# Performance work log

Measured on AMD Instinct MI355X. Metric: run time of the kernel, lower is better.

Reference implementation:

```python
import jax, jax.numpy as jnp
import numpy as np

B, S, D, H = 8, 2048, 1024, 1024

def setup_inputs() -> dict:
    key = jax.random.key(0)
    ks = jax.random.split(key, 7)
    scale = 1.0 / np.sqrt(D)
    x = jax.random.normal(ks[0], (B, S, D), dtype=jnp.float32)
    W_q = jax.random.uniform(ks[1], (H, D), jnp.float32, -scale, scale)
    b_q = jax.random.uniform(ks[2], (H,), jnp.float32, -scale, scale)
    W_k = jax.random.uniform(ks[3], (H, D), jnp.float32, -scale, scale)
    b_k = jax.random.uniform(ks[4], (H,), jnp.float32, -scale, scale)
    W_v = jax.random.uniform(ks[5], (H, D), jnp.float32, -scale, scale)
    b_v = jax.random.uniform(ks[6], (H,), jnp.float32, -scale, scale)
    return {"x": x, "W_q": W_q, "b_q": b_q, "W_k": W_k, "b_k": b_k, "W_v": W_v, "b_v": b_v}

def reference(x, W_q, b_q, W_k, b_k, W_v, b_v):
    # Linear layers: y = x @ W.T + b (torch nn.Linear convention)
    q = jnp.einsum('bsd,hd->bsh', x, W_q) + b_q
    k = jnp.einsum('bsd,hd->bsh', x, W_k) + b_k
    v = jnp.einsum('bsd,hd->bsh', x, W_v) + b_v
    score = jnp.einsum('bqh,bkh->bqk', q, k) / jnp.sqrt(jnp.float32(H))
    causal = jnp.tril(jnp.ones((S, S), dtype=bool))  # lower-triangular mask
    score = jnp.where(causal, score, jnp.float32(-1e9))
    attn = jax.nn.softmax(score, axis=-1)
    return jnp.einsum('bqk,bkh->bqh', attn, v)
```

## Files before the change

kernel.cpp:

```cpp
#include <hip/hip_runtime.h>
#include <hip/hip_bf16.h>
#include <cstdint>

#define BB 8
#define SS 2048
#define DD 1024
#define HH 1024

typedef __bf16 bf16x8 __attribute__((ext_vector_type(8)));
typedef float f32x4 __attribute__((ext_vector_type(4)));

#define AS1C(p) ((const __attribute__((address_space(1))) void*)(p))
#define AS3(p)  ((__attribute__((address_space(3))) void*)(p))

__device__ __forceinline__ float bf2f(uint16_t h) {
  union { uint32_t u; float f; } v; v.u = ((uint32_t)h) << 16; return v.f;
}
__device__ __forceinline__ uint16_t f2bf(float f) {
  union { float f; uint32_t u; } v; v.f = f;
  uint32_t u = v.u;
  return (uint16_t)((u + 0x7FFFu + ((u >> 16) & 1u)) >> 16);
}

__global__ void cvt_f32_bf16(const float* __restrict__ src,
                             uint16_t* __restrict__ dst, int n) {
  int i = (blockIdx.x * blockDim.x + threadIdx.x) * 8;
  const int stride = gridDim.x * blockDim.x * 8;
  for (; i < n; i += stride) {
    float4 f0 = *(const float4*)(src + i);
    float4 f1 = *(const float4*)(src + i + 4);
    alignas(16) uint16_t o[8];
    o[0] = f2bf(f0.x); o[1] = f2bf(f0.y); o[2] = f2bf(f0.z); o[3] = f2bf(f0.w);
    o[4] = f2bf(f1.x); o[5] = f2bf(f1.y); o[6] = f2bf(f1.z); o[7] = f2bf(f1.w);
    *(uint4*)(dst + i) = *(const uint4*)o;
  }
}

__global__ void cvt3_f32_bf16(const float* __restrict__ s0, const float* __restrict__ s1,
                              const float* __restrict__ s2, uint16_t* __restrict__ d0,
                              uint16_t* __restrict__ d1, uint16_t* __restrict__ d2, int n) {
  const float* src = (blockIdx.y == 0) ? s0 : (blockIdx.y == 1) ? s1 : s2;
  uint16_t* dst = (blockIdx.y == 0) ? d0 : (blockIdx.y == 1) ? d1 : d2;
  int i = (blockIdx.x * blockDim.x + threadIdx.x) * 8;
  const int stride = gridDim.x * blockDim.x * 8;
  for (; i < n; i += stride) {
    float4 f0 = *(const float4*)(src + i);
    float4 f1 = *(const float4*)(src + i + 4);
    alignas(16) uint16_t o[8];
    o[0] = f2bf(f0.x); o[1] = f2bf(f0.y); o[2] = f2bf(f0.z); o[3] = f2bf(f0.w);
    o[4] = f2bf(f1.x); o[5] = f2bf(f1.y); o[6] = f2bf(f1.z); o[7] = f2bf(f1.w);
    *(uint4*)(dst + i) = *(const uint4*)o;
  }
}

template <int MODE>
__launch_bounds__(256, 2)
__global__ void gemm_bt(const uint16_t* __restrict__ Aroot,
                        const uint16_t* __restrict__ Broot,
                        const float* __restrict__ bias,
                        void* __restrict__ Croot) {
  constexpr int K   = (MODE == 3) ? 2048 : 1024;
  constexpr int LDA = (MODE == 3) ? 2048 : 1024;
  constexpr int LDB = (MODE == 3) ? 2048 : 1024;
  constexpr int LDC = (MODE == 2) ? 2048 : 1024;

  const int tm = blockIdx.x, tn = blockIdx.y;
  if constexpr (MODE == 2) { if (tn > tm) return; }

  const uint16_t* A = Aroot;
  const uint16_t* Bp = Broot;
  uint16_t* C16 = (uint16_t*)Croot;
  float*    C32 = (float*)Croot;
  if constexpr (MODE == 2) {
    size_t z = blockIdx.z;
    A  += z * (size_t)(SS * DD);
    Bp += z * (size_t)(SS * DD);
    C16 += z * (size_t)SS * (size_t)SS;
  }
  if constexpr (MODE == 3) {
    size_t z = blockIdx.z;
    A  += z * (size_t)SS * (size_t)SS;
    Bp += z * (size_t)(HH * SS);
    C32 += z * (size_t)(SS * HH);
  }

  const int m0 = tm * 128, n0 = tn * 128;
  int kmax = K;
  if constexpr (MODE == 3) {
    kmax = (tm + 1) * 128;
    if (kmax > K) kmax = K;
  }

  __shared__ uint16_t As[128 * 32];
  __shared__ uint16_t Bs[128 * 32];

  const int tid  = threadIdx.x;
  const int lane = tid & 63;
  const int wv   = tid >> 6;
  const int wm   = (wv & 1) * 64;
  const int wn   = (wv >> 1) * 64;

  f32x4 acc[4][4];
#pragma unroll
  for (int i = 0; i < 4; i++)
#pragma unroll
    for (int j = 0; j < 4; j++)
#pragma unroll
      for (int e = 0; e < 4; e++) acc[i][j][e] = 0.f;

  const int lrow = lane >> 2;
  const int lcol = (lane & 3) * 8;
  const int r0   = wv * 32;

  const uint16_t* gA = A + (size_t)(m0 + r0 + lrow) * LDA + lcol;
  const uint16_t* gB = Bp + (size_t)(n0 + r0 + lrow) * LDB + lcol;

  const int fr = lane & 15;
  const int fk = (lane >> 4) * 8;

  for (int k0 = 0; k0 < kmax; k0 += 32) {
    __syncthreads();
    __builtin_amdgcn_global_load_lds(AS1C(gA + k0), AS3(&As[r0 * 32]), 16, 0, 0);
    __builtin_amdgcn_global_load_lds(AS1C(gA + k0 + 16 * LDA), AS3(&As[(r0 + 16) * 32]), 16, 0, 0);
    __builtin_amdgcn_global_load_lds(AS1C(gB + k0), AS3(&Bs[r0 * 32]), 16, 0, 0);
    __builtin_amdgcn_global_load_lds(AS1C(gB + k0 + 16 * LDB), AS3(&Bs[(r0 + 16) * 32]), 16, 0, 0);
    __syncthreads();

    bf16x8 af[4], bfr[4];
#pragma unroll
    for (int i = 0; i < 4; i++) {
      uint4 t = *(const uint4*)&As[(wm + i * 16 + fr) * 32 + fk];
      af[i] = __builtin_bit_cast(bf16x8, t);
    }
#pragma unroll
    for (int j = 0; j < 4; j++) {
      uint4 t = *(const uint4*)&Bs[(wn + j * 16 + fr) * 32 + fk];
      bfr[j] = __builtin_bit_cast(bf16x8, t);
    }
#pragma unroll
    for (int i = 0; i < 4; i++)
#pragma unroll
      for (int j = 0; j < 4; j++)
        acc[i][j] = __builtin_amdgcn_mfma_f32_16x16x32_bf16(af[i], bfr[j], acc[i][j], 0, 0, 0);
  }

  const int cr = (lane >> 4) * 4;
  const int cc = lane & 15;
#pragma unroll
  for (int i = 0; i < 4; i++) {
#pragma unroll
    for (int j = 0; j < 4; j++) {
      const int row0 = m0 + wm + i * 16 + cr;
      const int col  = n0 + wn + j * 16 + cc;
      float badd = 0.f;
      if constexpr (MODE == 0 || MODE == 1) badd = bias[col];
#pragma unroll
      for (int e = 0; e < 4; e++) {
        float x = acc[i][j][e] + badd;
        if constexpr (MODE == 2) x *= 0.03125f;
        const int r = row0 + e;
        if constexpr (MODE == 1) {
          const int bz = r >> 11;
          const int s  = r & (SS - 1);
          C16[(size_t)bz * (HH * SS) + (size_t)col * SS + s] = f2bf(x);
        } else if constexpr (MODE == 3) {
          C32[(size_t)r * LDC + col] = x;
        } else {
          C16[(size_t)r * LDC + col] = f2bf(x);
        }
      }
    }
  }
}

__launch_bounds__(256)
__global__ void softmax_causal(uint16_t* __restrict__ Sb) {
  const int rgl = blockIdx.x;
  const int b = rgl >> 11;
  const int i = rgl & (SS - 1);
  uint16_t* row = Sb + (size_t)b * SS * SS + (size_t)i * SS;
  const int t = threadIdx.x;
  const int base = t * 8;

  uint4 u = *(const uint4*)(row + base);
  const uint16_t* hs = (const uint16_t*)&u;
  float x[8];
  float lmax = -3.0e38f;
#pragma unroll
  for (int e = 0; e < 8; e++) {
    float f = bf2f(hs[e]);
    x[e] = (base + e <= i) ? f : -3.0e38f;
    lmax = fmaxf(lmax, x[e]);
  }
#pragma unroll
  for (int off = 32; off > 0; off >>= 1)
    lmax = fmaxf(lmax, __shfl_down(lmax, off));

  __shared__ float red[8];
  if ((t & 63) == 0) red[t >> 6] = lmax;
  __syncthreads();
  const float m = fmaxf(fmaxf(red[0], red[1]), fmaxf(red[2], red[3]));

  float lsum = 0.f;
#pragma unroll
  for (int e = 0; e < 8; e++) {
    float p = (base + e <= i) ? __expf(x[e] - m) : 0.f;
    x[e] = p;
    lsum += p;
  }
#pragma unroll
  for (int off = 32; off > 0; off >>= 1) lsum += __shfl_down(lsum, off);
  if ((t & 63) == 0) red[4 + (t >> 6)] = lsum;
  __syncthreads();
  const float inv = 1.f / (red[4] + red[5] + red[6] + red[7]);

  alignas(16) uint16_t o[8];
#pragma unroll
  for (int e = 0; e < 8; e++) o[e] = f2bf(x[e] * inv);
  *(uint4*)(row + base) = *(const uint4*)o;
}

extern "C" void kernel_launch(void* const* d_in, const int* in_sizes, int n_in,
                              void* d_out, int out_size, void* d_ws, size_t ws_size,
                              hipStream_t stream) {
  const float* x  = (const float*)d_in[0];
  const float* Wq = (const float*)d_in[1];
  const float* bq = (const float*)d_in[2];
  const float* Wk = (const float*)d_in[3];
  const float* bk = (const float*)d_in[4];
  const float* Wv = (const float*)d_in[5];
  const float* bv = (const float*)d_in[6];

  uint16_t* ws = (uint16_t*)d_ws;
  const size_t QKV = (size_t)BB * SS * HH;
  uint16_t* Q  = ws;
  uint16_t* Kp = ws + QKV;
  uint16_t* Vt = ws + 2 * QKV;
  uint16_t* Sb = ws + 3 * QKV;
  uint16_t* xb  = Sb;
  uint16_t* Wqb = Sb + QKV;
  uint16_t* Wkb = Wqb + (size_t)HH * DD;
  uint16_t* Wvb = Wkb + (size_t)HH * DD;

  dim3 blk(256);
  const int nx = BB * SS * DD;
  const int nw = HH * DD;
  cvt_f32_bf16<<<dim3(nx / 2048), blk, 0, stream>>>(x, xb, nx);
  cvt3_f32_bf16<<<dim3(nw / 2048, 3), blk, 0, stream>>>(Wq, Wk, Wv, Wqb, Wkb, Wvb, nw);

  dim3 gproj(BB * SS / 128, HH / 128);
  gemm_bt<0><<<gproj, blk, 0, stream>>>(xb, Wqb, bq, Q);
  gemm_bt<0><<<gproj, blk, 0, stream>>>(xb, Wkb, bk, Kp);
  gemm_bt<1><<<gproj, blk, 0, stream>>>(xb, Wvb, bv, Vt);
  gemm_bt<2><<<dim3(SS / 128, SS / 128, BB), blk, 0, stream>>>(Q, Kp, nullptr, Sb);
  softmax_causal<<<dim3(BB * SS), blk, 0, stream>>>(Sb);
  gemm_bt<3><<<dim3(SS / 128, HH / 128, BB), blk, 0, stream>>>(Sb, Vt, nullptr, d_out);
}
```

Baseline: 445.5 us.

## Fuse QKV projections into one GEMM launch and process K in 64-wide steps

The three separate Q/K/V projection GEMMs become a single launch over a 3x wider N grid, which relies on Wq, Wk and Wv being contiguous in the workspace and picks the bias and output layout per tile. The GEMM main loop now stages two 32-wide K slices per barrier pair into separate LDS buffers, halving the number of synchronisations. This is meant to cut launch overhead, fill the GPU better in the projection phase and reduce barrier stalls, at the cost of more LDS per block, which may lower occupancy. It also depends on every kmax being a multiple of 64, which holds for these shapes.

Result: faster. 434.5 us (-2.5%).

```diff
diff --git a/kernel.cpp b/kernel.cpp
--- a/kernel.cpp
+++ b/kernel.cpp
@@ -57,20 +57,23 @@
 __launch_bounds__(256, 2)
 __global__ void gemm_bt(const uint16_t* __restrict__ Aroot,
                         const uint16_t* __restrict__ Broot,
-                        const float* __restrict__ bias,
-                        void* __restrict__ Croot) {
+                        const float* __restrict__ bq,
+                        const float* __restrict__ bk,
+                        const float* __restrict__ bv,
+                        void* __restrict__ out0,
+                        uint16_t* __restrict__ out1,
+                        uint16_t* __restrict__ out2) {
   constexpr int K   = (MODE == 3) ? 2048 : 1024;
   constexpr int LDA = (MODE == 3) ? 2048 : 1024;
   constexpr int LDB = (MODE == 3) ? 2048 : 1024;
-  constexpr int LDC = (MODE == 2) ? 2048 : 1024;
 
   const int tm = blockIdx.x, tn = blockIdx.y;
   if constexpr (MODE == 2) { if (tn > tm) return; }
 
   const uint16_t* A = Aroot;
   const uint16_t* Bp = Broot;
-  uint16_t* C16 = (uint16_t*)Croot;
-  float*    C32 = (float*)Croot;
+  uint16_t* C16 = (uint16_t*)out0;
+  float*    C32 = (float*)out0;
   if constexpr (MODE == 2) {
     size_t z = blockIdx.z;
     A  += z * (size_t)(SS * DD);
@@ -91,8 +94,10 @@
     if (kmax > K) kmax = K;
   }
 
-  __shared__ uint16_t As[128 * 32];
-  __shared__ uint16_t Bs[128 * 32];
+  __shared__ uint16_t As0[128 * 32];
+  __shared__ uint16_t As1[128 * 32];
+  __shared__ uint16_t Bs0[128 * 32];
+  __shared__ uint16_t Bs1[128 * 32];
 
   const int tid  = threadIdx.x;
   const int lane = tid & 63;
@@ -118,55 +123,89 @@
   const int fr = lane & 15;
   const int fk = (lane >> 4) * 8;
 
-  for (int k0 = 0; k0 < kmax; k0 += 32) {
+  for (int k0 = 0; k0 < kmax; k0 += 64) {
     __syncthreads();
-    __builtin_amdgcn_global_load_lds(AS1C(gA + k0), AS3(&As[r0 * 32]), 16, 0, 0);
-    __builtin_amdgcn_global_load_lds(AS1C(gA + k0 + 16 * LDA), AS3(&As[(r0 + 16) * 32]), 16, 0, 0);
-    __builtin_amdgcn_global_load_lds(AS1C(gB + k0), AS3(&Bs[r0 * 32]), 16, 0, 0);
-    __builtin_amdgcn_global_load_lds(AS1C(gB + k0 + 16 * LDB), AS3(&Bs[(r0 + 16) * 32]), 16, 0, 0);
+    __builtin_amdgcn_global_load_lds(AS1C(gA + k0), AS3(&As0[r0 * 32]), 16, 0, 0);
+    __builtin_amdgcn_global_load_lds(AS1C(gA + k0 + 16 * LDA), AS3(&As0[(r0 + 16) * 32]), 16, 0, 0);
+    __builtin_amdgcn_global_load_lds(AS1C(gA + k0 + 32), AS3(&As1[r0 * 32]), 16, 0, 0);
+    __builtin_amdgcn_global_load_lds(AS1C(gA + k0 + 32 + 16 * LDA), AS3(&As1[(r0 + 16) * 32]), 16, 0, 0);
+    __builtin_amdgcn_global_load_lds(AS1C(gB + k0), AS3(&Bs0[r0 * 32]), 16, 0, 0);
+    __builtin_amdgcn_global_load_lds(AS1C(gB + k0 + 16 * LDB), AS3(&Bs0[(r0 + 16) * 32]), 16, 0, 0);
+    __builtin_amdgcn_global_load_lds(AS1C(gB + k0 + 32), AS3(&Bs1[r0 * 32]), 16, 0, 0);
+    __builtin_amdgcn_global_load_lds(AS1C(gB + k0 + 32 + 16 * LDB), AS3(&Bs1[(r0 + 16) * 32]), 16, 0, 0);
     __syncthreads();
 
     bf16x8 af[4], bfr[4];
 #pragma unroll
-    for (int i = 0; i < 4; i++) {
-      uint4 t = *(const uint4*)&As[(wm + i * 16 + fr) * 32 + fk];
-      af[i] = __builtin_bit_cast(bf16x8, t);
-    }
-#pragma unroll
-    for (int j = 0; j < 4; j++) {
-      uint4 t = *(const uint4*)&Bs[(wn + j * 16 + fr) * 32 + fk];
-      bfr[j] = __builtin_bit_cast(bf16x8, t);
-    }
+    for (int i = 0; i < 4; i++)
+      af[i] = __builtin_bit_cast(bf16x8, *(const uint4*)&As0[(wm + i * 16 + fr) * 32 + fk]);
+#pragma unroll
+    for (int j = 0; j < 4; j++)
+      bfr[j] = __builtin_bit_cast(bf16x8, *(const uint4*)&Bs0[(wn + j * 16 + fr) * 32 + fk]);
 #pragma unroll
     for (int i = 0; i < 4; i++)
 #pragma unroll
       for (int j = 0; j < 4; j++)
         acc[i][j] = __builtin_amdgcn_mfma_f32_16x16x32_bf16(af[i], bfr[j], acc[i][j], 0, 0, 0);
+
+#pragma unroll
+    for (int i = 0; i < 4; i++)
+      af[i] = __builtin_bit_cast(bf16x8, *(const uint4*)&As1[(wm + i * 16 + fr) * 32 + fk]);
+#pragma unroll
+    for (int j = 0; j < 4; j++)
+      bfr[j] = __builtin_bit_cast(bf16x8, *(const uint4*)&Bs1[(wn + j * 16 + fr) * 32 + fk]);
+#pragma unroll
+    for (int i = 0; i < 4; i++)
+#pragma unroll
+      for (int j = 0; j < 4; j++)
+        acc[i][j] = __builtin_amdgcn_mfma_f32_16x16x32_bf16(af[i], bfr[j], acc[i][j], 0, 0, 0);
   }
 
   const int cr = (lane >> 4) * 4;
   const int cc = lane & 15;
-#pragma unroll
-  for (int i = 0; i < 4; i++) {
-#pragma unroll
-    for (int j = 0; j < 4; j++) {
-      const int row0 = m0 + wm + i * 16 + cr;
-      const int col  = n0 + wn + j * 16 + cc;
-      float badd = 0.f;
-      if constexpr (MODE == 0 || MODE == 1) badd = bias[col];
-#pragma unroll
-      for (int e = 0; e < 4; e++) {
-        float x = acc[i][j][e] + badd;
-        if constexpr (MODE == 2) x *= 0.03125f;
-        const int r = row0 + e;
-        if constexpr (MODE == 1) {
-          const int bz = r >> 11;
-          const int s  = r & (SS - 1);
-          C16[(size_t)bz * (HH * SS) + (size_t)col * SS + s] = f2bf(x);
-        } else if constexpr (MODE == 3) {
-          C32[(size_t)r * LDC + col] = x;
-        } else {
-          C16[(size_t)r * LDC + col] = f2bf(x);
+
+  if constexpr (MODE == 0) {
+    const int sel   = n0 >> 10;
+    const int nloc0 = n0 & 1023;
+    const float* __restrict__ bsel = (sel == 0) ? bq : (sel == 1) ? bk : bv;
+    uint16_t* __restrict__ oQK = (sel == 1) ? out1 : (uint16_t*)out0;
+#pragma unroll
+    for (int i = 0; i < 4; i++) {
+#pragma unroll
+      for (int j = 0; j < 4; j++) {
+        const int row0 = m0 + wm + i * 16 + cr;
+        const int coll = nloc0 + wn + j * 16 + cc;
+        const float badd = bsel[coll];
+#pragma unroll
+        for (int e = 0; e < 4; e++) {
+          const float x = acc[i][j][e] + badd;
+          const int r = row0 + e;
+          if (sel == 2) {
+            const int bz = r >> 11;
+            const int s  = r & (SS - 1);
+            out2[(size_t)bz * (HH * SS) + (size_t)coll * SS + s] = f2bf(x);
+          } else {
+            oQK[(size_t)r * HH + coll] = f2bf(x);
+          }
+        }
+      }
+    }
+  } else {
+#pragma unroll
+    for (int i = 0; i < 4; i++) {
+#pragma unroll
+      for (int j = 0; j < 4; j++) {
+        const int row0 = m0 + wm + i * 16 + cr;
+        const int col  = n0 + wn + j * 16 + cc;
+#pragma unroll
+        for (int e = 0; e < 4; e++) {
+          float x = acc[i][j][e];
+          const int r = row0 + e;
+          if constexpr (MODE == 2) {
+            C16[(size_t)r * SS + col] = f2bf(x * 0.03125f);
+          } else {
+            C32[(size_t)r * HH + col] = x;
+          }
         }
       }
     }
@@ -248,11 +287,11 @@
   cvt_f32_bf16<<<dim3(nx / 2048), blk, 0, stream>>>(x, xb, nx);
   cvt3_f32_bf16<<<dim3(nw / 2048, 3), blk, 0, stream>>>(Wq, Wk, Wv, Wqb, Wkb, Wvb, nw);
 
-  dim3 gproj(BB * SS / 128, HH / 128);
-  gemm_bt<0><<<gproj, blk, 0, stream>>>(xb, Wqb, bq, Q);
-  gemm_bt<0><<<gproj, blk, 0, stream>>>(xb, Wkb, bk, Kp);
-  gemm_bt<1><<<gproj, blk, 0, stream>>>(xb, Wvb, bv, Vt);
-  gemm_bt<2><<<dim3(SS / 128, SS / 128, BB), blk, 0, stream>>>(Q, Kp, nullptr, Sb);
+  gemm_bt<0><<<dim3(BB * SS / 128, 3 * HH / 128), blk, 0, stream>>>(
+      xb, Wqb, bq, bk, bv, Q, Kp, Vt);
+  gemm_bt<2><<<dim3(SS / 128, SS / 128, BB), blk, 0, stream>>>(
+      Q, Kp, nullptr, nullptr, nullptr, Sb, nullptr, nullptr);
   softmax_causal<<<dim3(BB * SS), blk, 0, stream>>>(Sb);
-  gemm_bt<3><<<dim3(SS / 128, HH / 128, BB), blk, 0, stream>>>(Sb, Vt, nullptr, d_out);
-}
+  gemm_bt<3><<<dim3(SS / 128, HH / 128, BB), blk, 0, stream>>>(
+      Sb, Vt, nullptr, nullptr, nullptr, d_out, nullptr, nullptr);
+}
```
